# Optimization experiments

Hardware: AMD Instinct MI355X
Metric: run time of the kernel (lower is better)

Reference implementation:

```python
import jax, jax.numpy as jnp
import numpy as np

K = 9  # 3x3 kernel taps

def conv2d(x, w, b):
    # stride 1, padding 1, NCHW / OIHW
    out = jax.lax.conv_general_dilated(x, w, (1, 1), ((1, 1), (1, 1)),
                                       dimension_numbers=('NCHW', 'OIHW', 'NCHW'))
    return out + b[None, :, None, None]

def deform_conv2d(x, offset, mask, w, b):
    # torchvision modulated deformable conv, kernel 3x3, stride 1, pad 1, dilation 1
    B, C, H, W = x.shape
    off = offset.reshape(B, K, 2, H, W)  # per-tap (dy, dx)
    ii = (jnp.arange(K) // 3).astype(x.dtype) - 1.0  # kernel row offset (pad=1)
    jj = (jnp.arange(K) % 3).astype(x.dtype) - 1.0   # kernel col offset
    hh = jnp.arange(H, dtype=x.dtype)[None, None, :, None]
    ww = jnp.arange(W, dtype=x.dtype)[None, None, None, :]
    py = hh + ii[None, :, None, None] + off[:, :, 0]  # [B,K,H,W] sample rows
    px = ww + jj[None, :, None, None] + off[:, :, 1]  # [B,K,H,W] sample cols

    y0 = jnp.floor(py); x0 = jnp.floor(px)
    dy = py - y0; dx = px - x0
    y0 = y0.astype(jnp.int32); x0 = x0.astype(jnp.int32)

    xf = x.reshape(B, C, H * W)

    def gather(yi, xi):
        valid = ((yi >= 0) & (yi < H) & (xi >= 0) & (xi < W)).astype(x.dtype)
        yc = jnp.clip(yi, 0, H - 1)
        xc = jnp.clip(xi, 0, W - 1)
        idx = (yc * W + xc).reshape(B, K * H * W)
        v = jax.vmap(lambda xb, ib: xb[:, ib])(xf, idx)  # [B,C,K*H*W]
        return v.reshape(B, C, K, H, W) * valid[:, None]

    v00 = gather(y0,     x0)
    v01 = gather(y0,     x0 + 1)
    v10 = gather(y0 + 1, x0)
    v11 = gather(y0 + 1, x0 + 1)

    dy = dy[:, None]; dx = dx[:, None]  # broadcast over channel dim
    val = (v00 * (1 - dy) * (1 - dx) + v01 * (1 - dy) * dx
           + v10 * dy * (1 - dx) + v11 * dy * dx)
    val = val * mask[:, None]  # sigmoid modulation, [B,1,K,H,W]

    out = jnp.einsum('ock,bckhw->bohw', w.reshape(w.shape[0], C, K), val)
    return out + b[None, :, None, None]

def setup_inputs() -> dict:
    key = jax.random.key(0)
    k1, k2, k3 = jax.random.split(key, 3)
    x = jax.random.normal(k1, (8, 3, 512, 512), dtype=jnp.float32)
    w_off = jax.random.normal(k2, (27, 3, 3, 3), dtype=jnp.float32) * 0.05
    b_off = jnp.zeros((27,), dtype=jnp.float32)
    w_def = jax.random.normal(k3, (3, 3, 3, 3), dtype=jnp.float32) * 0.1
    b_def = jnp.zeros((3,), dtype=jnp.float32)
    return {'x': x, 'w_off': w_off, 'b_off': b_off, 'w_def': w_def, 'b_def': b_def}

def reference(x, w_off, b_off, w_def, b_def):
    ow = conv2d(x, w_off, b_off)            # [B,27,H,W]
    offset = ow[:, :18]                      # 2*9 offsets
    mask = jax.nn.sigmoid(ow[:, 18:])        # 9 modulation masks
    return deform_conv2d(x, offset, mask, w_def, b_def)
```

## Files before the change

kernel.cpp:

```cpp
#include <hip/hip_runtime.h>
#include <math.h>

typedef float f2 __attribute__((ext_vector_type(2)));
typedef float f2u __attribute__((ext_vector_type(2), aligned(4)));

#define BN 8
#define CIN 3
#define HH 512
#define WW 512
#define KK 9
#define PATCH 27
#define TAPBLK 96

__global__ void reorder_weights(const float* __restrict__ w_off,
                                const float* __restrict__ w_def,
                                float* __restrict__ ws)
{
    for (int idx = threadIdx.x; idx < KK * TAPBLK; idx += blockDim.x) {
        const int k = idx / TAPBLK;
        const int r = idx % TAPBLK;
        float v = 0.0f;
        if (r < 56) {
            const int q = r >> 1, half = r & 1;
            if (q < PATCH) v = w_off[(2 * k + half) * PATCH + q];
        } else if (r < 84) {
            const int i = r - 56;
            if (i < PATCH) v = w_off[(18 + k) * PATCH + i];
        } else {
            const int j = r - 84;
            const int c = j >> 2, o = j & 3;
            if (o < 3) v = w_def[o * PATCH + c * KK + k];
        }
        ws[idx] = v;
    }
}

__global__ __launch_bounds__(256) void deform_fused_kernel(
    const float* __restrict__ x,
    const float* __restrict__ wsw,
    const float* __restrict__ b_off,
    const float* __restrict__ b_def,
    float* __restrict__ out)
{
    const int w = blockIdx.x * blockDim.x + threadIdx.x;
    const int h = blockIdx.y;
    const int b = blockIdx.z;

    const size_t plane = (size_t)HH * WW;
    const float* xb = x + (size_t)b * CIN * plane;

    float patch[28];
    patch[27] = 0.0f;
    #pragma unroll
    for (int c = 0; c < CIN; ++c) {
        const float* xp = xb + c * plane;
        #pragma unroll
        for (int t = 0; t < KK; ++t) {
            const int yy = h + t / 3 - 1;
            const int xx = w + t % 3 - 1;
            const bool in = (yy >= 0) & (yy < HH) & (xx >= 0) & (xx < WW);
            patch[c * KK + t] = in ? xp[yy * WW + xx] : 0.0f;
        }
    }

    const float hf = (float)h;
    const float wf = (float)w;

    float acc0 = b_def[0];
    float acc1 = b_def[1];
    float acc2 = b_def[2];

    float oy, ox, om;
    {
        const float* blk = wsw;
        float a0 = b_off[0], a1 = b_off[1], s = b_off[18];
        #pragma unroll
        for (int q = 0; q < 28; ++q) {
            a0 = fmaf(blk[2 * q],     patch[q], a0);
            a1 = fmaf(blk[2 * q + 1], patch[q], a1);
        }
        #pragma unroll
        for (int i = 0; i < 28; ++i) {
            s = fmaf(blk[56 + i], patch[i], s);
        }
        oy = a0; ox = a1; om = s;
    }

    #pragma unroll 1
    for (int k = 1; k <= KK; ++k) {
        const int kp = k - 1;
        const float* blkp = wsw + kp * TAPBLK;

        const float cw00 = blkp[84], cw01 = blkp[85], cw02 = blkp[86];
        const float cw10 = blkp[88], cw11 = blkp[89], cw12 = blkp[90];
        const float cw20 = blkp[92], cw21 = blkp[93], cw22 = blkp[94];

        const float m = 1.0f / (1.0f + __expf(-om));

        const float py = hf + (float)(kp / 3 - 1) + oy;
        const float px = wf + (float)(kp % 3 - 1) + ox;
        const float y0f = floorf(py);
        const float x0f = floorf(px);
        const float dy = py - y0f;
        const float dx = px - x0f;
        const int y0 = (int)y0f;
        const int x0 = (int)x0f;

        const float omdy = 1.0f - dy;
        const float omdx = 1.0f - dx;
        const float w00 = omdx * omdy;
        const float w01 = dx * omdy;
        const float w10 = omdx * dy;
        const float w11 = dx * dy;

        const int interior = (y0 >= 0) & (y0 + 1 < HH) & (x0 >= 0) & (x0 + 1 < WW);

        f2 vT0, vB0, vT1, vB1, vT2, vB2;
        if (__all(interior)) {
            const int idx = y0 * WW + x0;
            const float* xp0 = xb + idx;
            const float* xp1 = xp0 + plane;
            const float* xp2 = xp1 + plane;
            vT0 = *(const f2u*)(xp0);  vB0 = *(const f2u*)(xp0 + WW);
            vT1 = *(const f2u*)(xp1);  vB1 = *(const f2u*)(xp1 + WW);
            vT2 = *(const f2u*)(xp2);  vB2 = *(const f2u*)(xp2 + WW);
        } else {
            const bool vy0 = (y0 >= 0)     & (y0 < HH);
            const bool vy1 = (y0 + 1 >= 0) & (y0 + 1 < HH);
            const bool vx0 = (x0 >= 0)     & (x0 < WW);
            const bool vx1 = (x0 + 1 >= 0) & (x0 + 1 < WW);

            const int yc0 = min(max(y0, 0), HH - 1);
            const int yc1 = min(max(y0 + 1, 0), HH - 1);
            const int xc0 = min(max(x0, 0), WW - 1);
            const int xc1 = min(max(x0 + 1, 0), WW - 1);

            const float* xp0 = xb;
            const float* xp1 = xp0 + plane;
            const float* xp2 = xp1 + plane;

            vT0.x = (vy0 & vx0) ? xp0[yc0 * WW + xc0] : 0.0f;
            vT0.y = (vy0 & vx1) ? xp0[yc0 * WW + xc1] : 0.0f;
            vB0.x = (vy1 & vx0) ? xp0[yc1 * WW + xc0] : 0.0f;
            vB0.y = (vy1 & vx1) ? xp0[yc1 * WW + xc1] : 0.0f;
            vT1.x = (vy0 & vx0) ? xp1[yc0 * WW + xc0] : 0.0f;
            vT1.y = (vy0 & vx1) ? xp1[yc0 * WW + xc1] : 0.0f;
            vB1.x = (vy1 & vx0) ? xp1[yc1 * WW + xc0] : 0.0f;
            vB1.y = (vy1 & vx1) ? xp1[yc1 * WW + xc1] : 0.0f;
            vT2.x = (vy0 & vx0) ? xp2[yc0 * WW + xc0] : 0.0f;
            vT2.y = (vy0 & vx1) ? xp2[yc0 * WW + xc1] : 0.0f;
            vB2.x = (vy1 & vx0) ? xp2[yc1 * WW + xc0] : 0.0f;
            vB2.y = (vy1 & vx1) ? xp2[yc1 * WW + xc1] : 0.0f;
        }

        if (k < KK) {
            const float* blk = wsw + k * TAPBLK;
            float a0 = b_off[2 * k], a1 = b_off[2 * k + 1], s = b_off[18 + k];
            #pragma unroll
            for (int q = 0; q < 28; ++q) {
                a0 = fmaf(blk[2 * q],     patch[q], a0);
                a1 = fmaf(blk[2 * q + 1], patch[q], a1);
            }
            #pragma unroll
            for (int i = 0; i < 28; ++i) {
                s = fmaf(blk[56 + i], patch[i], s);
            }
            oy = a0; ox = a1; om = s;
        }

        {
            float v0 = vT0.x * w00;
            v0 = fmaf(vT0.y, w01, v0);
            v0 = fmaf(vB0.x, w10, v0);
            v0 = fmaf(vB0.y, w11, v0);
            const float val0 = v0 * m;

            float v1 = vT1.x * w00;
            v1 = fmaf(vT1.y, w01, v1);
            v1 = fmaf(vB1.x, w10, v1);
            v1 = fmaf(vB1.y, w11, v1);
            const float val1 = v1 * m;

            float v2 = vT2.x * w00;
            v2 = fmaf(vT2.y, w01, v2);
            v2 = fmaf(vB2.x, w10, v2);
            v2 = fmaf(vB2.y, w11, v2);
            const float val2 = v2 * m;

            acc0 = fmaf(cw00, val0, acc0);
            acc1 = fmaf(cw01, val0, acc1);
            acc2 = fmaf(cw02, val0, acc2);
            acc0 = fmaf(cw10, val1, acc0);
            acc1 = fmaf(cw11, val1, acc1);
            acc2 = fmaf(cw12, val1, acc2);
            acc0 = fmaf(cw20, val2, acc0);
            acc1 = fmaf(cw21, val2, acc1);
            acc2 = fmaf(cw22, val2, acc2);
        }
    }

    const size_t base = (size_t)b * (CIN * plane) + (size_t)h * WW + w;
    out[base]             = acc0;
    out[base + plane]     = acc1;
    out[base + 2 * plane] = acc2;
}

extern "C" void kernel_launch(void* const* d_in, const int* in_sizes, int n_in,
                              void* d_out, int out_size, void* d_ws, size_t ws_size,
                              hipStream_t stream) {
    const float* x     = (const float*)d_in[0];
    const float* w_off = (const float*)d_in[1];
    const float* b_off = (const float*)d_in[2];
    const float* w_def = (const float*)d_in[3];
    const float* b_def = (const float*)d_in[4];
    float* out = (float*)d_out;
    float* wsw = (float*)d_ws;

    reorder_weights<<<1, 256, 0, stream>>>(w_off, w_def, wsw);

    dim3 block(256, 1, 1);
    dim3 grid(WW / 256, HH, BN);
    deform_fused_kernel<<<grid, block, 0, stream>>>(x, wsw, b_off, b_def, out);
}
```

Baseline: 182.0 us.

## Stage a 5-row input window in shared memory for patch and bilinear gathers

Each block now cooperatively loads a 3x5x260 input halo window into LDS, zero-filled outside the image. The 3x3 patch reads for the offset conv come from that window, and so do the bilinear gathers whenever every lane's sample falls inside it. Otherwise the code falls back to the existing clamped global path. This replaces many redundant global/L2 loads with LDS reads, at the cost of about 15.6 KB of shared memory per block, which may limit occupancy, plus a __syncthreads barrier.

After: 191.6 us. 1.05x slower.

```diff
diff --git a/kernel.cpp b/kernel.cpp
--- a/kernel.cpp
+++ b/kernel.cpp
@@ -11,6 +11,9 @@
 #define KK 9
 #define PATCH 27
 #define TAPBLK 96
+#define WROWS 5
+#define WCOLS 260
+#define XSN (CIN * WROWS * WCOLS)
 
 __global__ void reorder_weights(const float* __restrict__ w_off,
                                 const float* __restrict__ w_def,
@@ -42,24 +45,41 @@
     const float* __restrict__ b_def,
     float* __restrict__ out)
 {
-    const int w = blockIdx.x * blockDim.x + threadIdx.x;
+    const int t = threadIdx.x;
+    const int wblk = blockIdx.x * 256;
+    const int w = wblk + t;
     const int h = blockIdx.y;
     const int b = blockIdx.z;
 
     const size_t plane = (size_t)HH * WW;
     const float* xb = x + (size_t)b * CIN * plane;
+
+    __shared__ float xs[XSN];
+    for (int e = t; e < XSN; e += 256) {
+        const int c = e / (WROWS * WCOLS);
+        const int rem = e % (WROWS * WCOLS);
+        const int r = rem / WCOLS;
+        const int ix = rem % WCOLS;
+        const int gy = h - 2 + r;
+        const int gx = wblk - 2 + ix;
+        float v = 0.0f;
+        if ((unsigned)gy < (unsigned)HH && (unsigned)gx < (unsigned)WW)
+            v = xb[(size_t)c * plane + gy * WW + gx];
+        xs[e] = v;
+    }
+    __syncthreads();
 
     float patch[28];
     patch[27] = 0.0f;
     #pragma unroll
     for (int c = 0; c < CIN; ++c) {
-        const float* xp = xb + c * plane;
         #pragma unroll
-        for (int t = 0; t < KK; ++t) {
-            const int yy = h + t / 3 - 1;
-            const int xx = w + t % 3 - 1;
-            const bool in = (yy >= 0) & (yy < HH) & (xx >= 0) & (xx < WW);
-            patch[c * KK + t] = in ? xp[yy * WW + xx] : 0.0f;
+        for (int rr = 0; rr < 3; ++rr) {
+            #pragma unroll
+            for (int cc = 0; cc < 3; ++cc) {
+                patch[c * KK + rr * 3 + cc] =
+                    xs[(c * WROWS + rr + 1) * WCOLS + (t + 1 + cc)];
+            }
         }
     }
 
@@ -113,17 +133,19 @@
         const float w10 = omdx * dy;
         const float w11 = dx * dy;
 
-        const int interior = (y0 >= 0) & (y0 + 1 < HH) & (x0 >= 0) & (x0 + 1 < WW);
+        const int iy  = y0 - h + 2;
+        const int ixw = x0 - wblk + 2;
+        const int win = ((unsigned)iy <= 3u) & ((unsigned)ixw <= 258u);
 
         f2 vT0, vB0, vT1, vB1, vT2, vB2;
-        if (__all(interior)) {
-            const int idx = y0 * WW + x0;
-            const float* xp0 = xb + idx;
-            const float* xp1 = xp0 + plane;
-            const float* xp2 = xp1 + plane;
-            vT0 = *(const f2u*)(xp0);  vB0 = *(const f2u*)(xp0 + WW);
-            vT1 = *(const f2u*)(xp1);  vB1 = *(const f2u*)(xp1 + WW);
-            vT2 = *(const f2u*)(xp2);  vB2 = *(const f2u*)(xp2 + WW);
+        if (__all(win)) {
+            const float* ps = &xs[iy * WCOLS + ixw];
+            vT0 = *(const f2u*)(ps);
+            vB0 = *(const f2u*)(ps + WCOLS);
+            vT1 = *(const f2u*)(ps + WROWS * WCOLS);
+            vB1 = *(const f2u*)(ps + WROWS * WCOLS + WCOLS);
+            vT2 = *(const f2u*)(ps + 2 * WROWS * WCOLS);
+            vB2 = *(const f2u*)(ps + 2 * WROWS * WCOLS + WCOLS);
         } else {
             const bool vy0 = (y0 >= 0)     & (y0 < HH);
             const bool vy1 = (y0 + 1 >= 0) & (y0 + 1 < HH);
```
